# Kernel optimization log

Measured on AMD Instinct MI355X. Metric: run time of the kernel, lower is better.

## Reference

```python
import jax, jax.numpy as jnp
import numpy as np

D_MODEL = 2048
NUM_HEADS = 16
HEAD_DIM = D_MODEL // NUM_HEADS
B, S = 2, 2048


def setup_inputs() -> dict:
    key = jax.random.key(0)
    ks = jax.random.split(key, 11)
    scale = 1.0 / np.sqrt(D_MODEL)
    inp = {
        "query": jax.random.normal(ks[0], (B, S, D_MODEL), dtype=jnp.float32),
        "key": jax.random.normal(ks[1], (B, S, D_MODEL), dtype=jnp.float32),
        "value": jax.random.normal(ks[2], (B, S, D_MODEL), dtype=jnp.float32),
        "Wq": jax.random.normal(ks[3], (D_MODEL, D_MODEL), dtype=jnp.float32) * scale,
        "bq": jax.random.normal(ks[4], (D_MODEL,), dtype=jnp.float32) * 0.01,
        "Wk": jax.random.normal(ks[5], (D_MODEL, D_MODEL), dtype=jnp.float32) * scale,
        "bk": jax.random.normal(ks[6], (D_MODEL,), dtype=jnp.float32) * 0.01,
        "Wv": jax.random.normal(ks[7], (D_MODEL, D_MODEL), dtype=jnp.float32) * scale,
        "bv": jax.random.normal(ks[8], (D_MODEL,), dtype=jnp.float32) * 0.01,
        "Wo": jax.random.normal(ks[9], (D_MODEL, D_MODEL), dtype=jnp.float32) * scale,
        "bo": jax.random.normal(ks[10], (D_MODEL,), dtype=jnp.float32) * 0.01,
    }
    return inp


def _shape(x, B, S):
    # [B, S, D] -> [B, H, S, hd]
    return x.reshape(B, S, NUM_HEADS, HEAD_DIM).transpose(0, 2, 1, 3)


def reference(query, key, value, Wq, bq, Wk, bk, Wv, bv, Wo, bo):
    B, Sq, D = query.shape
    Sk = key.shape[1]
    # Linear layers (torch: y = x @ W.T + b)
    Q = _shape(query @ Wq.T + bq, B, Sq)   # [B,H,Sq,hd]
    K = _shape(key @ Wk.T + bk, B, Sk)     # [B,H,Sk,hd]
    V = _shape(value @ Wv.T + bv, B, Sk)   # [B,H,Sk,hd]
    scores = jnp.einsum('bhqd,bhkd->bhqk', Q, K) / jnp.sqrt(jnp.float32(HEAD_DIM))
    # causal mask: triu(ones(Sq, Sk), diagonal=1)
    causal = jnp.triu(jnp.ones((Sq, Sk), dtype=bool), k=1)
    scores = jnp.where(causal[None, None, :, :], jnp.float32(-jnp.inf), scores)
    attn = jax.nn.softmax(scores, axis=-1)
    out = jnp.einsum('bhqk,bhkd->bhqd', attn, V)
    out = out.transpose(0, 2, 1, 3).reshape(B, Sq, D)
    return out @ Wo.T + bo
```

## Files before the change

### kernel.cpp

```cpp
#include <hip/hip_runtime.h>
#include <hip/hip_bf16.h>

typedef __attribute__((ext_vector_type(8))) short short8;
typedef __attribute__((ext_vector_type(4))) short s16x4;
typedef __attribute__((ext_vector_type(4))) float f32x4;

#define MFMA_BF16(A, B, C) __builtin_amdgcn_mfma_f32_16x16x32_bf16(A, B, C, 0, 0, 0)

__device__ __forceinline__ void gload_lds16(const __hip_bfloat16* g, __hip_bfloat16* l) {
  __builtin_amdgcn_global_load_lds(
      (const __attribute__((address_space(1))) unsigned int*)g,
      (__attribute__((address_space(3))) unsigned int*)l, 16, 0, 0);
}

__device__ __forceinline__ float finite_or(float x, float repl) {
  unsigned u;
  __builtin_memcpy(&u, &x, 4);
  return ((u & 0x7f800000u) == 0x7f800000u) ? repl : x;
}

__device__ __forceinline__ short bf16_bits(float x) {
  __hip_bfloat16 b = __float2bfloat16(x);
  short s;
  __builtin_memcpy(&s, &b, 2);
  return s;
}

__device__ __forceinline__ short8 pack8(f32x4 a, f32x4 b) {
  short8 r;
  r[0] = bf16_bits(a[0]); r[1] = bf16_bits(a[1]);
  r[2] = bf16_bits(a[2]); r[3] = bf16_bits(a[3]);
  r[4] = bf16_bits(b[0]); r[5] = bf16_bits(b[1]);
  r[6] = bf16_bits(b[2]); r[7] = bf16_bits(b[3]);
  return r;
}

__global__ __launch_bounds__(256) void cvt_kernel(
    const float* x0, const float* x1, const float* x2,
    const float* w0, const float* w1, const float* w2, const float* w3,
    __hip_bfloat16* y0, __hip_bfloat16* y1, __hip_bfloat16* y2,
    __hip_bfloat16* u0, __hip_bfloat16* u1, __hip_bfloat16* u2, __hip_bfloat16* u3)
{
  const int z = blockIdx.y;
  const float* s = z == 0 ? x0 : z == 1 ? x1 : z == 2 ? x2
                 : z == 3 ? w0 : z == 4 ? w1 : z == 5 ? w2 : w3;
  __hip_bfloat16* d = z == 0 ? y0 : z == 1 ? y1 : z == 2 ? y2
                    : z == 3 ? u0 : z == 4 ? u1 : z == 5 ? u2 : u3;
  const size_t n = (z < 3) ? (size_t)8388608 : (size_t)4194304;
  const size_t stride = (size_t)gridDim.x * 256 * 8;
  for (size_t i = ((size_t)blockIdx.x * 256 + threadIdx.x) * 8; i < n; i += stride) {
    f32x4 a = *(const f32x4*)(s + i);
    f32x4 b = *(const f32x4*)(s + i + 4);
    *(short8*)((short*)d + i) = pack8(a, b);
  }
}

#define GBUF 24576

__device__ __forceinline__ void stage_A(const __hip_bfloat16* Ab, __hip_bfloat16* bufA,
                                        int kcol, int t, int wave) {
#pragma unroll
  for (int r = 0; r < 2; ++r) {
    const int ci = r * 512 + t;
    const int row = ci >> 3, c = ci & 7;
    const int sc = c ^ (row & 7);
    gload_lds16(Ab + (size_t)row * 2048 + kcol + sc * 8, bufA + r * 4096 + wave * 512);
  }
}
__device__ __forceinline__ void stage_Br(const __hip_bfloat16* Bb, __hip_bfloat16* bufB,
                                         int kcol, int t, int wave, int r) {
  const int ci = r * 512 + t;
  const int row = ci >> 3, c = ci & 7;
  const int sc = c ^ (row & 7);
  gload_lds16(Bb + (size_t)row * 2048 + kcol + sc * 8, bufB + r * 4096 + wave * 512);
}

template <typename OutT>
__device__ __forceinline__ void gemm8p_body(
    const __hip_bfloat16* __restrict__ A, const __hip_bfloat16* __restrict__ Bt,
    const float* __restrict__ bias, OutT* __restrict__ C,
    float trip, __hip_bfloat16* sm)
{
  constexpr int K = 2048, N = 2048, NT = K / 64;
  const int t = threadIdx.x, wave = t >> 6, lane = t & 63;
  const int ll = lane & 15, lg = lane >> 4;
  const int wmB = (wave >> 2) * 64, wnB = (wave & 3) * 64;
  const int m0 = blockIdx.y * 128, n0 = blockIdx.x * 256;
  const __hip_bfloat16* Ab = A + (size_t)m0 * K;
  const __hip_bfloat16* Bb = Bt + (size_t)n0 * K;

  f32x4 acc[4][4] = {};

  stage_A(Ab, sm, 0, t, wave);
  stage_Br(Bb, sm + 8192, 0, t, wave, 0);
  stage_Br(Bb, sm + 8192, 0, t, wave, 1);
  stage_Br(Bb, sm + 8192, 0, t, wave, 2);
  stage_Br(Bb, sm + 8192, 0, t, wave, 3);
  stage_A(Ab, sm + GBUF, 64, t, wave);
  stage_Br(Bb, sm + GBUF + 8192, 64, t, wave, 0);
  stage_Br(Bb, sm + GBUF + 8192, 64, t, wave, 1);
  stage_Br(Bb, sm + GBUF + 8192, 64, t, wave, 2);
  stage_Br(Bb, sm + GBUF + 8192, 64, t, wave, 3);
  asm volatile("s_waitcnt vmcnt(6)" ::: "memory");
  __builtin_amdgcn_s_barrier();

  for (int i = 0; i < NT; ++i) {
    const __hip_bfloat16* bufA = sm + (i % 3) * GBUF;
    const __hip_bfloat16* bufB = bufA + 8192;
    const bool pf = (i + 2 < NT);
    __hip_bfloat16* pA = sm + ((i + 2) % 3) * GBUF;
    const int pk = (i + 2) * 64;

#pragma unroll
    for (int kk = 0; kk < 2; ++kk) {
      short8 af[4], bf[4];
#pragma unroll
      for (int f = 0; f < 4; ++f) {
        const int ar = wmB + f * 16 + ll;
        af[f] = *(const short8*)&bufA[ar * 64 + (((kk * 4 + lg) ^ (ar & 7)) << 3)];
        const int br = wnB + f * 16 + ll;
        bf[f] = *(const short8*)&bufB[br * 64 + (((kk * 4 + lg) ^ (br & 7)) << 3)];
      }
      if (pf) {
        if (kk == 0) {
          stage_A(Ab, pA, pk, t, wave);
          stage_Br(Bb, pA + 8192, pk, t, wave, 0);
        } else {
          stage_Br(Bb, pA + 8192, pk, t, wave, 1);
          stage_Br(Bb, pA + 8192, pk, t, wave, 2);
          stage_Br(Bb, pA + 8192, pk, t, wave, 3);
        }
      }
      asm volatile("s_waitcnt lgkmcnt(0)" ::: "memory");
      __builtin_amdgcn_sched_barrier(0);
      __builtin_amdgcn_s_setprio(1);
#pragma unroll
      for (int mi = 0; mi < 4; ++mi)
#pragma unroll
        for (int ni = 0; ni < 4; ++ni)
          acc[mi][ni] = MFMA_BF16(af[mi], bf[ni], acc[mi][ni]);
      __builtin_amdgcn_s_setprio(0);
      __builtin_amdgcn_sched_barrier(0);
    }

    const int rem = NT - 1 - i;
    if (rem >= 2) {
      asm volatile("s_waitcnt vmcnt(6)" ::: "memory");
      __builtin_amdgcn_s_barrier();
    } else if (rem == 1) {
      asm volatile("s_waitcnt vmcnt(0)" ::: "memory");
      __builtin_amdgcn_s_barrier();
    }
  }

#pragma unroll
  for (int mi = 0; mi < 4; ++mi)
#pragma unroll
    for (int ni = 0; ni < 4; ++ni) {
      const int col = n0 + wnB + ni * 16 + ll;
      const float bv = bias[col];
#pragma unroll
      for (int j = 0; j < 4; ++j) {
        const int row = m0 + wmB + mi * 16 + lg * 4 + j;
        const float val = finite_or(acc[mi][ni][j] + bv, trip);
        if constexpr (__is_same(OutT, float))
          C[(size_t)row * N + col] = val;
        else
          C[(size_t)row * N + col] = __float2bfloat16(val);
      }
    }
}

__global__ __launch_bounds__(512) void gemm_qkv_kernel(
    const __hip_bfloat16* xq, const __hip_bfloat16* xk, const __hip_bfloat16* xv,
    const __hip_bfloat16* Wq, const __hip_bfloat16* Wk, const __hip_bfloat16* Wv,
    const float* bq, const float* bk, const float* bv,
    __hip_bfloat16* Q, __hip_bfloat16* K, __hip_bfloat16* V)
{
  __shared__ __align__(16) __hip_bfloat16 sm[3 * GBUF];
  const int z = blockIdx.z;
  const __hip_bfloat16* X = z == 0 ? xq : (z == 1 ? xk : xv);
  const __hip_bfloat16* W = z == 0 ? Wq : (z == 1 ? Wk : Wv);
  const float*          B = z == 0 ? bq : (z == 1 ? bk : bv);
  __hip_bfloat16*       O = z == 0 ? Q  : (z == 1 ? K  : V);
  gemm8p_body<__hip_bfloat16>(X, W, B, O, 20000.0f, sm);
}

__global__ __launch_bounds__(512) void gemm_out_kernel(
    const __hip_bfloat16* A, const __hip_bfloat16* W, const float* b, float* C)
{
  __shared__ __align__(16) __hip_bfloat16 sm[3 * GBUF];
  gemm8p_body<float>(A, W, b, C, 50000.0f, sm);
}

__global__ __launch_bounds__(256) void transpose_v_kernel(
    const __hip_bfloat16* __restrict__ V, __hip_bfloat16* __restrict__ Vt)
{
  __shared__ __align__(16) __hip_bfloat16 tile[32][33];
  const int bh = blockIdx.z;
  const int b = bh >> 4, h = bh & 15;
  const int s0 = blockIdx.x * 32, d0 = blockIdx.y * 32;
  const int x = threadIdx.x, y = threadIdx.y;
#pragma unroll
  for (int k = 0; k < 32; k += 8)
    tile[y + k][x] = V[(size_t)(b * 2048 + s0 + y + k) * 2048 + h * 128 + d0 + x];
  __syncthreads();
#pragma unroll
  for (int k = 0; k < 32; k += 8)
    Vt[(size_t)(bh * 128 + d0 + y + k) * 2048 + s0 + x] = tile[x][y + k];
}

__global__ __launch_bounds__(256) void attn_kernel(
    const __hip_bfloat16* __restrict__ Qb, const __hip_bfloat16* __restrict__ Kb,
    const __hip_bfloat16* __restrict__ Vt, __hip_bfloat16* __restrict__ Ob)
{
  constexpr int S = 2048, D = 2048, HD = 128;
  __shared__ __align__(16) __hip_bfloat16 Ks[2][64 * 128];
  __shared__ __align__(16) __hip_bfloat16 Vs[2][128 * 64];
  __shared__ __align__(16) short Ps[4][16 * 64];

  const int t = threadIdx.x, wave = t >> 6, lane = t & 63;
  const int lg = lane >> 4, ll = lane & 15;
  const int bh = blockIdx.y;
  const int b = bh >> 4, h = bh & 15;
  char* const Psw = (char*)&Ps[wave][0];

  auto stageKV = [&](int buf, int kv0) {
#pragma unroll
    for (int r = 0; r < 4; ++r) {
      const int s = r * 256 + t;
      const int row = s >> 4, ch = s & 15;
      const int sc = ch ^ (row & 7);
      gload_lds16(Kb + (size_t)(b * S + kv0 + row) * D + h * HD + sc * 8,
                  &Ks[buf][0] + r * 2048 + wave * 512);
    }
#pragma unroll
    for (int r = 0; r < 4; ++r) {
      const int s = r * 256 + t;
      const int d = s >> 3, ch = s & 7;
      const int sc = ch ^ (d & 7);
      gload_lds16(Vt + (size_t)(bh * HD + d) * S + kv0 + sc * 8,
                  &Vs[buf][0] + r * 2048 + wave * 512);
    }
  };

  for (int ph = 0; ph < 2; ++ph) {
    const int qi = (ph == 0) ? (int)blockIdx.x : 31 - (int)blockIdx.x;
    const int q0 = qi * 64;
    const int qrow = q0 + wave * 16 + ll;

    short8 qf[4];
    const __hip_bfloat16* qptr = Qb + (size_t)(b * S + qrow) * D + h * HD + lg * 8;
#pragma unroll
    for (int kc = 0; kc < 4; ++kc) qf[kc] = *(const short8*)(qptr + kc * 32);

    f32x4 oacc[8] = {};
    float mrun = -1e30f, lrun = 0.f;

    __builtin_amdgcn_s_barrier();
    stageKV(0, 0);

    for (int tk = 0; tk <= qi; ++tk) {
      const int cur = tk & 1, nxt = cur ^ 1;
      __builtin_amdgcn_s_barrier();
      const bool pf = (tk < qi);
      if (pf) stageKV(nxt, (tk + 1) * 64);
      if (pf) asm volatile("s_waitcnt vmcnt(8)" ::: "memory");
      else    asm volatile("s_waitcnt vmcnt(0)" ::: "memory");
      __builtin_amdgcn_s_barrier();

      const int kv0 = tk * 64;
      const __hip_bfloat16* Kc = &Ks[cur][0];
      const __hip_bfloat16* Vc = &Vs[cur][0];

      f32x4 sacc[4] = {};
#pragma unroll
      for (int nf = 0; nf < 4; ++nf) {
        const int krow = nf * 16 + ll;
#pragma unroll
        for (int kc = 0; kc < 4; ++kc) {
          const int sw = (kc * 4 + lg) ^ (krow & 7);
          const short8 kf = *(const short8*)&Kc[krow * 128 + sw * 8];
          sacc[nf] = MFMA_BF16(kf, qf[kc], sacc[nf]);
        }
      }

      float sv[4][4];
      float mx = -1e30f;
#pragma unroll
      for (int nf = 0; nf < 4; ++nf)
#pragma unroll
        for (int j = 0; j < 4; ++j) {
          float s = sacc[nf][j] * 0.08838834764831845f;
          if (kv0 + nf * 16 + lg * 4 + j > qrow) s = -1e30f;
          sv[nf][j] = s;
          mx = fmaxf(mx, s);
        }
      mx = fmaxf(mx, __shfl_xor(mx, 16));
      mx = fmaxf(mx, __shfl_xor(mx, 32));
      const float mnew = fmaxf(mrun, mx);
      const float alpha = __expf(mrun - mnew);
      mrun = mnew;

      float rs = 0.f;
#pragma unroll
      for (int nf = 0; nf < 4; ++nf) {
        s16x4 pk;
#pragma unroll
        for (int j = 0; j < 4; ++j) {
          const float p = __expf(sv[nf][j] - mnew);
          rs += p;
          pk[j] = bf16_bits(p);
        }
        const int chunk = (nf * 2 + (lg >> 1)) ^ (ll & 7);
        *(s16x4*)(Psw + ll * 128 + chunk * 16 + (lg & 1) * 8) = pk;
      }
      rs += __shfl_xor(rs, 16);
      rs += __shfl_xor(rs, 32);
      lrun = lrun * alpha + rs;
#pragma unroll
      for (int df = 0; df < 8; ++df)
#pragma unroll
        for (int j = 0; j < 4; ++j) oacc[df][j] *= alpha;

      asm volatile("s_waitcnt lgkmcnt(0)" ::: "memory");
      __builtin_amdgcn_sched_barrier(0);

#pragma unroll
      for (int ks = 0; ks < 2; ++ks) {
        const int pchunk = (ks * 4 + lg) ^ (ll & 7);
        const short8 pf8 = *(const short8*)(Psw + ll * 128 + pchunk * 16);
#pragma unroll
        for (int df = 0; df < 8; ++df) {
          const int vrow = df * 16 + ll;
          const int sw = (ks * 4 + lg) ^ (vrow & 7);
          const short8 vf = *(const short8*)&Vc[vrow * 64 + sw * 8];
          oacc[df] = MFMA_BF16(vf, pf8, oacc[df]);
        }
      }
    }

    const float inv = 1.0f / lrun;
#pragma unroll
    for (int df = 0; df < 8; ++df) {
      s16x4 o;
#pragma unroll
      for (int j = 0; j < 4; ++j)
        o[j] = bf16_bits(finite_or(oacc[df][j] * inv, 300.0f));
      *(s16x4*)(Ob + (size_t)(b * S + qrow) * D + h * HD + df * 16 + lg * 4) = o;
    }
  }
}

extern "C" void kernel_launch(void* const* d_in, const int* in_sizes, int n_in,
                              void* d_out, int out_size, void* d_ws, size_t ws_size,
                              hipStream_t stream)
{
  const float* q  = (const float*)d_in[0];
  const float* k  = (const float*)d_in[1];
  const float* v  = (const float*)d_in[2];
  const float* Wq = (const float*)d_in[3];
  const float* bq = (const float*)d_in[4];
  const float* Wk = (const float*)d_in[5];
  const float* bk = (const float*)d_in[6];
  const float* Wv = (const float*)d_in[7];
  const float* bv = (const float*)d_in[8];
  const float* Wo = (const float*)d_in[9];
  const float* bo = (const float*)d_in[10];

  char* wsb = (char*)d_ws;
  const size_t MB = 1024 * 1024;
  __hip_bfloat16* Qw  = (__hip_bfloat16*)(wsb + 0 * MB);
  __hip_bfloat16* Kw  = (__hip_bfloat16*)(wsb + 16 * MB);
  __hip_bfloat16* Vw  = (__hip_bfloat16*)(wsb + 32 * MB);
  __hip_bfloat16* xqb = (__hip_bfloat16*)(wsb + 48 * MB);
  __hip_bfloat16* xkb = (__hip_bfloat16*)(wsb + 64 * MB);
  __hip_bfloat16* xvb = (__hip_bfloat16*)(wsb + 80 * MB);
  __hip_bfloat16* Wqb = (__hip_bfloat16*)(wsb + 96 * MB);
  __hip_bfloat16* Wkb = (__hip_bfloat16*)(wsb + 104 * MB);
  __hip_bfloat16* Wvb = (__hip_bfloat16*)(wsb + 112 * MB);
  __hip_bfloat16* Wob = (__hip_bfloat16*)(wsb + 120 * MB);
  __hip_bfloat16* Vtw = xqb;
  __hip_bfloat16* Ow  = xkb;

  cvt_kernel<<<dim3(1024, 7), 256, 0, stream>>>(
      q, k, v, Wq, Wk, Wv, Wo, xqb, xkb, xvb, Wqb, Wkb, Wvb, Wob);
  gemm_qkv_kernel<<<dim3(8, 32, 3), 512, 0, stream>>>(
      xqb, xkb, xvb, Wqb, Wkb, Wvb, bq, bk, bv, Qw, Kw, Vw);
  transpose_v_kernel<<<dim3(64, 4, 32), dim3(32, 8), 0, stream>>>(Vw, Vtw);
  attn_kernel<<<dim3(16, 32), 256, 0, stream>>>(Qw, Kw, Vtw, Ow);
  gemm_out_kernel<<<dim3(8, 32), 512, 0, stream>>>(
      Ow, Wob, bo, (float*)d_out);
}
```

Measured before the change: 290.7 us.

## Compute V projection directly transposed to eliminate separate V transpose kernel

The V projection is now computed as Wv · xv^T, a GEMM with M=2048 (feature dim) and N=4096 (batch*seq) and a per-row bias, so it writes V already transposed into the layout the attention kernel wants. The standalone transpose kernel and its extra read/write of V through memory are removed, and the attention kernel's V address is adjusted to the new [h*hd, b*S] layout. In exchange the V GEMM now runs as a separate launch instead of sharing the QKV launch, which may lower overlap and occupancy across the three projections.

```diff
diff --git a/kernel.cpp b/kernel.cpp
--- a/kernel.cpp
+++ b/kernel.cpp
@@ -75,13 +75,13 @@
   gload_lds16(Bb + (size_t)row * 2048 + kcol + sc * 8, bufB + r * 4096 + wave * 512);
 }
 
-template <typename OutT>
+template <typename OutT, bool BIAS_ROW>
 __device__ __forceinline__ void gemm8p_body(
     const __hip_bfloat16* __restrict__ A, const __hip_bfloat16* __restrict__ Bt,
     const float* __restrict__ bias, OutT* __restrict__ C,
-    float trip, __hip_bfloat16* sm)
-{
-  constexpr int K = 2048, N = 2048, NT = K / 64;
+    int N, float trip, __hip_bfloat16* sm)
+{
+  constexpr int K = 2048, NT = K / 64;
   const int t = threadIdx.x, wave = t >> 6, lane = t & 63;
   const int ll = lane & 15, lg = lane >> 4;
   const int wmB = (wave >> 2) * 64, wnB = (wave & 3) * 64;
@@ -158,10 +158,11 @@
 #pragma unroll
     for (int ni = 0; ni < 4; ++ni) {
       const int col = n0 + wnB + ni * 16 + ll;
-      const float bv = bias[col];
+      const float bcol = BIAS_ROW ? 0.f : bias[col];
 #pragma unroll
       for (int j = 0; j < 4; ++j) {
         const int row = m0 + wmB + mi * 16 + lg * 4 + j;
+        const float bv = BIAS_ROW ? bias[row] : bcol;
         const float val = finite_or(acc[mi][ni][j] + bv, trip);
         if constexpr (__is_same(OutT, float))
           C[(size_t)row * N + col] = val;
@@ -172,42 +173,33 @@
 }
 
 __global__ __launch_bounds__(512) void gemm_qkv_kernel(
-    const __hip_bfloat16* xq, const __hip_bfloat16* xk, const __hip_bfloat16* xv,
-    const __hip_bfloat16* Wq, const __hip_bfloat16* Wk, const __hip_bfloat16* Wv,
-    const float* bq, const float* bk, const float* bv,
-    __hip_bfloat16* Q, __hip_bfloat16* K, __hip_bfloat16* V)
+    const __hip_bfloat16* xq, const __hip_bfloat16* xk,
+    const __hip_bfloat16* Wq, const __hip_bfloat16* Wk,
+    const float* bq, const float* bk,
+    __hip_bfloat16* Q, __hip_bfloat16* K)
 {
   __shared__ __align__(16) __hip_bfloat16 sm[3 * GBUF];
   const int z = blockIdx.z;
-  const __hip_bfloat16* X = z == 0 ? xq : (z == 1 ? xk : xv);
-  const __hip_bfloat16* W = z == 0 ? Wq : (z == 1 ? Wk : Wv);
-  const float*          B = z == 0 ? bq : (z == 1 ? bk : bv);
-  __hip_bfloat16*       O = z == 0 ? Q  : (z == 1 ? K  : V);
-  gemm8p_body<__hip_bfloat16>(X, W, B, O, 20000.0f, sm);
+  const __hip_bfloat16* X = z == 0 ? xq : xk;
+  const __hip_bfloat16* W = z == 0 ? Wq : Wk;
+  const float*          B = z == 0 ? bq : bk;
+  __hip_bfloat16*       O = z == 0 ? Q  : K;
+  gemm8p_body<__hip_bfloat16, false>(X, W, B, O, 2048, 20000.0f, sm);
+}
+
+__global__ __launch_bounds__(512) void gemm_vt_kernel(
+    const __hip_bfloat16* Wv, const __hip_bfloat16* xv,
+    const float* bv, __hip_bfloat16* Vt2)
+{
+  __shared__ __align__(16) __hip_bfloat16 sm[3 * GBUF];
+  gemm8p_body<__hip_bfloat16, true>(Wv, xv, bv, Vt2, 4096, 30000.0f, sm);
 }
 
 __global__ __launch_bounds__(512) void gemm_out_kernel(
     const __hip_bfloat16* A, const __hip_bfloat16* W, const float* b, float* C)
 {
   __shared__ __align__(16) __hip_bfloat16 sm[3 * GBUF];
-  gemm8p_body<float>(A, W, b, C, 50000.0f, sm);
-}
-
-__global__ __launch_bounds__(256) void transpose_v_kernel(
-    const __hip_bfloat16* __restrict__ V, __hip_bfloat16* __restrict__ Vt)
-{
-  __shared__ __align__(16) __hip_bfloat16 tile[32][33];
-  const int bh = blockIdx.z;
-  const int b = bh >> 4, h = bh & 15;
-  const int s0 = blockIdx.x * 32, d0 = blockIdx.y * 32;
-  const int x = threadIdx.x, y = threadIdx.y;
-#pragma unroll
-  for (int k = 0; k < 32; k += 8)
-    tile[y + k][x] = V[(size_t)(b * 2048 + s0 + y + k) * 2048 + h * 128 + d0 + x];
-  __syncthreads();
-#pragma unroll
-  for (int k = 0; k < 32; k += 8)
-    Vt[(size_t)(bh * 128 + d0 + y + k) * 2048 + s0 + x] = tile[x][y + k];
+  gemm8p_body<float, false>(A, W, b, C, 2048, 50000.0f, sm);
 }
 
 __global__ __launch_bounds__(256) void attn_kernel(
@@ -239,7 +231,7 @@
       const int s = r * 256 + t;
       const int d = s >> 3, ch = s & 7;
       const int sc = ch ^ (d & 7);
-      gload_lds16(Vt + (size_t)(bh * HD + d) * S + kv0 + sc * 8,
+      gload_lds16(Vt + (size_t)(h * HD + d) * (2 * S) + b * S + kv0 + sc * 8,
                   &Vs[buf][0] + r * 2048 + wave * 512);
     }
   };
@@ -372,7 +364,7 @@
   const size_t MB = 1024 * 1024;
   __hip_bfloat16* Qw  = (__hip_bfloat16*)(wsb + 0 * MB);
   __hip_bfloat16* Kw  = (__hip_bfloat16*)(wsb + 16 * MB);
-  __hip_bfloat16* Vw  = (__hip_bfloat16*)(wsb + 32 * MB);
+  __hip_bfloat16* Vt2 = (__hip_bfloat16*)(wsb + 32 * MB);
   __hip_bfloat16* xqb = (__hip_bfloat16*)(wsb + 48 * MB);
   __hip_bfloat16* xkb = (__hip_bfloat16*)(wsb + 64 * MB);
   __hip_bfloat16* xvb = (__hip_bfloat16*)(wsb + 80 * MB);
@@ -380,15 +372,14 @@
   __hip_bfloat16* Wkb = (__hip_bfloat16*)(wsb + 104 * MB);
   __hip_bfloat16* Wvb = (__hip_bfloat16*)(wsb + 112 * MB);
   __hip_bfloat16* Wob = (__hip_bfloat16*)(wsb + 120 * MB);
-  __hip_bfloat16* Vtw = xqb;
   __hip_bfloat16* Ow  = xkb;
 
   cvt_kernel<<<dim3(1024, 7), 256, 0, stream>>>(
       q, k, v, Wq, Wk, Wv, Wo, xqb, xkb, xvb, Wqb, Wkb, Wvb, Wob);
-  gemm_qkv_kernel<<<dim3(8, 32, 3), 512, 0, stream>>>(
-      xqb, xkb, xvb, Wqb, Wkb, Wvb, bq, bk, bv, Qw, Kw, Vw);
-  transpose_v_kernel<<<dim3(64, 4, 32), dim3(32, 8), 0, stream>>>(Vw, Vtw);
-  attn_kernel<<<dim3(16, 32), 256, 0, stream>>>(Qw, Kw, Vtw, Ow);
+  gemm_qkv_kernel<<<dim3(8, 32, 2), 512, 0, stream>>>(
+      xqb, xkb, Wqb, Wkb, bq, bk, Qw, Kw);
+  gemm_vt_kernel<<<dim3(16, 16), 512, 0, stream>>>(Wvb, xvb, bv, Vt2);
+  attn_kernel<<<dim3(16, 32), 256, 0, stream>>>(Qw, Kw, Vt2, Ow);
   gemm_out_kernel<<<dim3(8, 32), 512, 0, stream>>>(
       Ow, Wob, bo, (float*)d_out);
 }
```

Result: no change. 288.5 us (-0.8%).
